# Kernel tuning notes

Measured on AMD Instinct MI355X. Metric: run time of the kernel, lower is better.

Reference implementation:

```python
import jax, jax.numpy as jnp
import numpy as np

B, N_PER, DEG = 1024, 256, 16
N = B * N_PER            # 262144 total nodes
E = B * N_PER * DEG      # 4194304 edges
F_IN, H, K, C = 7, 64, 50, 2


def setup_inputs() -> dict:
    key = jax.random.key(0)
    ks = jax.random.split(key, 16)
    rng = np.random.default_rng(0)
    # within-graph random edges: nodes of graph g occupy [g*N_PER, (g+1)*N_PER)
    offs = np.repeat(np.arange(B, dtype=np.int64) * N_PER, N_PER * DEG)
    src = offs + rng.integers(0, N_PER, size=E)
    dst = offs + rng.integers(0, N_PER, size=E)
    edge_index = jnp.asarray(np.stack([src, dst]), dtype=jnp.int64)
    batch = jnp.repeat(jnp.arange(B, dtype=jnp.int64), N_PER)
    sc = lambda fan: 1.0 / np.sqrt(fan)
    return {
        'x': jax.random.normal(ks[0], (N, F_IN), jnp.float32),
        'W1a': jax.random.normal(ks[1], (F_IN, H), jnp.float32) * sc(F_IN),
        'b1a': jnp.zeros((H,), jnp.float32),
        'W1b': jax.random.normal(ks[2], (H, H), jnp.float32) * sc(H),
        'b1b': jnp.zeros((H,), jnp.float32),
        'Wp': jax.random.normal(ks[3], (H, K), jnp.float32) * sc(H),
        'bp': jnp.zeros((K,), jnp.float32),
        'W2a': jax.random.normal(ks[4], (H, H), jnp.float32) * sc(H),
        'b2a': jnp.zeros((H,), jnp.float32),
        'W2b': jax.random.normal(ks[5], (H, H), jnp.float32) * sc(H),
        'b2b': jnp.zeros((H,), jnp.float32),
        'Wl': jax.random.normal(ks[6], (H, C), jnp.float32) * sc(H),
        'bl': jnp.zeros((C,), jnp.float32),
        'edge_index': edge_index,
        'batch': batch,
    }


def reference(x, W1a, b1a, W1b, b1b, Wp, bp, W2a, b2a, W2b, b2b, Wl, bl,
              edge_index, batch):
    src, dst = edge_index[0], edge_index[1]
    # --- sparse GINConv (eps=0): MLP(x + sum_{j in N(i)} x_j) ---
    agg = jnp.zeros_like(x).at[dst].add(x[src])          # scatter-add over edges
    h = jax.nn.relu((x + agg) @ W1a + b1a) @ W1b + b1b   # [N, H]
    # --- densify per graph (equal-size contiguous graphs) ---
    xd = h.reshape(B, N_PER, H)                          # [B, n, H]
    g = src // N_PER
    si = src % N_PER
    di = dst % N_PER
    A = jnp.zeros((B, N_PER, N_PER), x.dtype).at[g, si, di].add(1.0)
    # --- BNPool-style soft cluster pooling ---
    S = jax.nn.softmax(xd @ Wp + bp, axis=-1)            # [B, n, K]
    xp = jnp.einsum('bnk,bnd->bkd', S, xd)               # [B, K, H]
    AS = jnp.einsum('bnm,bmk->bnk', A, S)
    Ap = jnp.einsum('bnk,bnl->bkl', S, AS)               # [B, K, K]
    SSt = jnp.einsum('bnk,bmk->bnm', S, S)
    link_loss = jnp.sqrt(jnp.sum((A - SSt) ** 2)) / A.size
    ent_loss = -jnp.mean(jnp.sum(S * jnp.log(S + 1e-15), axis=-1))
    aux_loss = link_loss + ent_loss
    # --- DenseGINConv (eps=0): MLP(x + A @ x) ---
    h2 = xp + jnp.einsum('bkl,bld->bkd', Ap, xp)
    h2 = jax.nn.relu(h2 @ W2a + b2a) @ W2b + b2b         # [B, K, H]
    # --- mean pool over clusters + classifier ---
    logits = h2.mean(axis=1) @ Wl + bl                   # [B, C]
    return jax.nn.log_softmax(logits, axis=-1), aux_loss
```

## Files before the change

### kernel.cpp

```cpp
#include <hip/hip_runtime.h>
#include <math.h>

#define NG   1024
#define NP   256
#define EPG  4096
#define ETOT 4194304
#define NTOT (NG * NP)
#define FIN  7
#define HD   64
#define KC   50
#define CHK  64
#define FST  72
#define TSC  0.00390625f
#define TSCI 256.0f

#define SW_ST(k, n)  ((k) * 256 + ((n) ^ (((k) & 7) << 3)))
#define SW_AW(r, w)  ((r) * 128 + ((w) ^ (((r) & 7) << 2)))
#define SW_AH(r, h)  ((r) * 256 + ((h) ^ (((r) & 7) << 3)))


typedef __attribute__((ext_vector_type(8))) _Float16 v8h;
typedef __attribute__((ext_vector_type(4))) float v4f;

__device__ __align__(16) _Float16 g_W1bT[HD * HD];
__device__ __align__(16) _Float16 g_WWT[HD * HD];
__device__ __align__(16) _Float16 g_W2aT[HD * HD];
__device__ __align__(16) _Float16 g_W2bT[HD * HD];
__device__ float g_bP[HD];

__global__ void kw_conv(const float* __restrict__ W1b, const float* __restrict__ Wp,
                        const float* __restrict__ W2a, const float* __restrict__ W2b,
                        const float* __restrict__ b1b, const float* __restrict__ bp,
                        float* __restrict__ ws) {
    const int b = blockIdx.x, tid = threadIdx.x;
    if (b == 0 && tid < 4) ws[tid] = 0.f;
    {
        int i = b * 256 + tid;
        int d = i >> 6, j = i & 63;
        g_W1bT[i] = (_Float16)W1b[j * HD + d];
        g_W2aT[i] = (_Float16)W2a[j * HD + d];
        g_W2bT[i] = (_Float16)W2b[j * HD + d];
    }
    {
        int k = b * 4 + (tid >> 6), j = tid & 63;
        float acc = 0.f;
        if (k < KC) {
            for (int d = 0; d < HD; ++d)
                acc += W1b[j * HD + d] * Wp[d * KC + k];
        }
        g_WWT[k * HD + j] = (_Float16)acc;
    }
    if (tid < 4) {
        int k = b * 4 + tid;
        float a = 0.f;
        if (k < KC) {
            for (int d = 0; d < HD; ++d) a += b1b[d] * Wp[d * KC + k];
            a += bp[k];
        }
        g_bP[k] = a;
    }
}

__global__ void finalize_k(const float* __restrict__ ws, float* __restrict__ out) {
    if (threadIdx.x == 0) {
        float num = ws[0] - 2.f * ws[2] + ws[3];
        float link = sqrtf(fmaxf(num, 0.f)) / 67108864.0f;
        float ent  = -ws[1] / 262144.0f;
        out[2048] = link + ent;
    }
}

__device__ __forceinline__ float blockReduceN(float v, float* red, int nw) {
    __syncthreads();
    #pragma unroll
    for (int o = 32; o > 0; o >>= 1) v += __shfl_down(v, o);
    if ((threadIdx.x & 63) == 0) red[threadIdx.x >> 6] = v;
    __syncthreads();
    float r = 0.f;
    if (threadIdx.x == 0) {
        for (int i = 0; i < nw; ++i) r += red[i];
    }
    return r;
}

__launch_bounds__(1024, 2)
__global__ void mega(const int* __restrict__ esrc, const int* __restrict__ edst,
                     const float* __restrict__ x,
                     const float* __restrict__ W1a, const float* __restrict__ b1a,
                     const float* __restrict__ b1b,
                     const float* __restrict__ b2a, const float* __restrict__ b2b,
                     const float* __restrict__ Wl,  const float* __restrict__ bl,
                     float* __restrict__ out, float* __restrict__ ws)
{
    __shared__ __align__(16) _Float16 ST[64 * 256];
    __shared__ __align__(16) unsigned char aux[9216];
    __shared__ __align__(16) union {
        struct {
            unsigned char ssi[EPG];
            float xt8[NP * 8];
            unsigned int hist[256], cur[256], roff[NP + 1];
        } k1;
        struct {
            _Float16 t1b[CHK * FST];
            _Float16 t1T[CHK * FST];
            _Float16 Pf[CHK * FST];
        } k2;
        struct {
            unsigned int cnt[64 * 128];
        } a;
        struct {
            _Float16 Apf_tf[64 * FST];
            _Float16 xpT[64 * FST];
            _Float16 h2f[64 * FST];
        } b;
    } u;
    __shared__ float cs[64];
    __shared__ float red[16];

    float* xagg = (float*)aux;
    _Float16* T1T = (_Float16*)aux;

    const int g = blockIdx.x, tid = threadIdx.x;
    const int lane = tid & 63, wid = tid >> 6;
    const int l15 = lane & 15, quad = lane >> 4, fko = quad * 8;
    const int mt = (wid >> 2) << 4, nt = (wid & 3) << 4;

    for (int i = tid; i < 64 * 128; i += 1024) ((unsigned int*)ST)[i] = 0u;
    if (tid < 256) u.k1.hist[tid] = 0u;
    __syncthreads();

    unsigned int cellr[4];
    #pragma unroll
    for (int j = 0; j < 4; ++j) {
        int e = tid + j * 1024;
        int s = esrc[g * EPG + e] & (NP - 1);
        int d = edst[g * EPG + e] & (NP - 1);
        cellr[j] = (unsigned)((s << 8) | d);
        atomicAdd(&u.k1.hist[d], 1u);
    }
    for (int i = tid; i < NP * 8; i += 1024) {
        int n = i >> 3, f = i & 7;
        u.k1.xt8[i] = (f < FIN) ? x[g * NP * FIN + n * FIN + f] : 0.f;
    }
    __syncthreads();

    if (wid == 0) {
        unsigned carry = 0;
        for (int c = 0; c < 4; ++c) {
            unsigned v = u.k1.hist[c * 64 + lane];
            unsigned s = v;
            #pragma unroll
            for (int o = 1; o < 64; o <<= 1) {
                unsigned t = __shfl_up(s, o);
                if (lane >= o) s += t;
            }
            unsigned excl = s - v + carry;
            u.k1.roff[c * 64 + lane] = excl;
            u.k1.cur[c * 64 + lane] = excl;
            carry += __shfl(s, 63);
        }
        if (lane == 0) u.k1.roff[NP] = EPG;
    }
    __syncthreads();

    #pragma unroll
    for (int j = 0; j < 4; ++j) {
        unsigned c = cellr[j];
        unsigned p2 = atomicAdd(&u.k1.cur[c & 255u], 1u);
        u.k1.ssi[p2] = (unsigned char)(c >> 8);
    }
    __syncthreads();

    {
        const int gi = tid >> 3, f = tid & 7;
        for (int n = gi; n < NP; n += 128) {
            int beg = u.k1.roff[n], end = u.k1.roff[n + 1];
            float a = u.k1.xt8[n * 8 + f];
            for (int e = beg; e < end; ++e)
                a += u.k1.xt8[u.k1.ssi[e] * 8 + f];
            xagg[n * 8 + f] = a;
        }
    }
    __syncthreads();

    float entL = 0.f;
    v4f spa = {0.f, 0.f, 0.f, 0.f};
    {
        float w1r[FIN];
        #pragma unroll
        for (int f = 0; f < FIN; ++f) w1r[f] = W1a[f * HD + lane];
        float b1r = b1a[lane];

        for (int ch2 = 0; ch2 < 4; ++ch2) {
            const int rb = ch2 * 64;
            for (int n = wid; n < CHK; n += 16) {
                float a = b1r;
                #pragma unroll
                for (int f = 0; f < FIN; ++f) a += xagg[(rb + n) * 8 + f] * w1r[f];
                _Float16 tv = (_Float16)fmaxf(a, 0.f);
                u.k2.t1b[n * FST + lane] = tv;
                u.k2.t1T[lane * FST + n] = tv;
            }
            __syncthreads();

            {
                v4f acc = {0.f, 0.f, 0.f, 0.f};
                #pragma unroll
                for (int ks = 0; ks < 2; ++ks) {
                    v8h af = *(const v8h*)&u.k2.t1b[(mt + l15) * FST + ks * 32 + fko];
                    v8h bf = *(const v8h*)&g_WWT[(nt + l15) * HD + ks * 32 + fko];
                    acc = __builtin_amdgcn_mfma_f32_16x16x32_f16(af, bf, acc, 0, 0, 0);
                }
                int kcol = nt + l15;
                if (kcol < KC) {
                    float bv = g_bP[kcol];
                    #pragma unroll
                    for (int r = 0; r < 4; ++r)
                        u.k2.Pf[(mt + quad * 4 + r) * FST + kcol] =
                            (_Float16)(acc[r] + bv);
                }
            }
            __syncthreads();

            for (int n = wid; n < CHK; n += 16) {
                float a = (lane < KC) ? (float)u.k2.Pf[n * FST + lane] : -INFINITY;
                float m = a;
                #pragma unroll
                for (int o = 32; o > 0; o >>= 1) m = fmaxf(m, __shfl_xor(m, o));
                float e = __expf(a - m);
                float ss = e;
                #pragma unroll
                for (int o = 32; o > 0; o >>= 1) ss += __shfl_xor(ss, o);
                float s = e / ss;
                if (lane < KC) {
                    ST[SW_ST(lane, rb + n)] = (_Float16)s;
                    entL += s * __logf(s + 1e-15f);
                }
            }
            __syncthreads();

            {
                const int ar = mt + l15, br = nt + l15;
                #pragma unroll
                for (int ks = 0; ks < 2; ++ks) {
                    v8h af = *(const v8h*)&ST[SW_ST(ar, rb + ks * 32 + fko)];
                    v8h bf = *(const v8h*)&u.k2.t1T[br * FST + ks * 32 + fko];
                    spa = __builtin_amdgcn_mfma_f32_16x16x32_f16(af, bf, spa, 0, 0, 0);
                }
            }
            __syncthreads();
        }
    }

    {
        _Float16* SPb = u.k2.t1b;
        int c = nt + l15;
        #pragma unroll
        for (int r = 0; r < 4; ++r)
            SPb[(mt + quad * 4 + r) * FST + c] = (_Float16)spa[r];
    }
    {
        int k = tid >> 4, q = tid & 15;
        float v = 0.f;
        #pragma unroll
        for (int i = 0; i < 16; ++i) v += (float)ST[SW_ST(k, q * 16 + i)];
        #pragma unroll
        for (int o = 8; o > 0; o >>= 1) v += __shfl_xor(v, o);
        if (q == 0) cs[k] = v;
    }
    {
        float rE = blockReduceN(entL, red, 16);
        if (tid == 0) atomicAdd(&ws[1], rE);
    }

    v4f axp;
    {
        const int d = nt + l15;
        float bv = b1b[d];
        #pragma unroll
        for (int r = 0; r < 4; ++r) axp[r] = cs[mt + quad * 4 + r] * bv;
        #pragma unroll
        for (int ks = 0; ks < 2; ++ks) {
            v8h af = *(const v8h*)&u.k2.t1b[(mt + l15) * FST + ks * 32 + fko];
            v8h bf = *(const v8h*)&g_W1bT[(nt + l15) * HD + ks * 32 + fko];
            axp = __builtin_amdgcn_mfma_f32_16x16x32_f16(af, bf, axp, 0, 0, 0);
        }
    }
    __syncthreads();

    float sumA2 = 0.f;
    v4f ap = {0.f, 0.f, 0.f, 0.f};
    v4f ag = {0.f, 0.f, 0.f, 0.f};

    for (int ch = 0; ch < 4; ++ch) {
        for (int i = tid; i < 64 * 128; i += 1024) u.a.cnt[i] = 0u;
        __syncthreads();

        int rlo = ch << 6;
        #pragma unroll
        for (int j = 0; j < 4; ++j) {
            unsigned c = cellr[j];
            int sr = (int)(c >> 8) - rlo;
            if ((unsigned)sr < 64u) {
                int d = c & 255u;
                atomicAdd(&u.a.cnt[SW_AW(sr, d >> 1)],
                          (d & 1) ? 0x10000u : 1u);
            }
        }
        __syncthreads();

        for (int i = tid; i < 64 * 128; i += 1024) {
            unsigned v = u.a.cnt[i];
            float m0 = (float)(v & 0xffffu), m1 = (float)(v >> 16);
            sumA2 += m0 * m0 + m1 * m1;
            union { unsigned uu; _Float16 h[2]; } cv;
            cv.h[0] = (_Float16)m0; cv.h[1] = (_Float16)m1;
            u.a.cnt[i] = cv.uu;
        }
        __syncthreads();

        const _Float16* Af = (const _Float16*)u.a.cnt;

        {
            const int ar = mt + l15, br = nt + l15;
            v4f acc = {0.f, 0.f, 0.f, 0.f};
            #pragma unroll
            for (int ks = 0; ks < 8; ++ks) {
                v8h af = *(const v8h*)&Af[SW_AH(ar, ks * 32 + fko)];
                v8h bf = *(const v8h*)&ST[SW_ST(br, ks * 32 + fko)];
                acc = __builtin_amdgcn_mfma_f32_16x16x32_f16(af, bf, acc, 0, 0, 0);
            }
            int c = nt + l15;
            #pragma unroll
            for (int r = 0; r < 4; ++r)
                T1T[c * FST + mt + quad * 4 + r] = (_Float16)acc[r];
        }
        __syncthreads();

        {
            const int ar = mt + l15, br = nt + l15;
            #pragma unroll
            for (int ks = 0; ks < 2; ++ks) {
                int ko = (ch << 6) + ks * 32 + fko;
                v8h af = *(const v8h*)&ST[SW_ST(ar, ko)];
                v8h bt = *(const v8h*)&T1T[br * FST + ks * 32 + fko];
                v8h bs = *(const v8h*)&ST[SW_ST(br, ko)];
                ap = __builtin_amdgcn_mfma_f32_16x16x32_f16(af, bt, ap, 0, 0, 0);
                ag = __builtin_amdgcn_mfma_f32_16x16x32_f16(af, bs, ag, 0, 0, 0);
            }
        }
        __syncthreads();
    }

    float tr = 0.f, g2 = 0.f;
    {
        int c = nt + l15;
        #pragma unroll
        for (int r = 0; r < 4; ++r) {
            int k = mt + quad * 4 + r;
            u.b.Apf_tf[k * FST + c] = (_Float16)ap[r];
            u.b.xpT[c * FST + k] = (_Float16)axp[r];
            if (k < KC && c < KC) {
                if (k == c) tr += ap[r];
                g2 += ag[r] * ag[r];
            }
        }
    }

    float rA = blockReduceN(sumA2, red, 16);
    float rT = blockReduceN(tr, red, 16);
    float rG = blockReduceN(g2, red, 16);
    if (tid == 0) {
        atomicAdd(&ws[0], rA);
        atomicAdd(&ws[2], rT);
        atomicAdd(&ws[3], rG);
    }
    __syncthreads();

    {
        v4f hacc = axp;
        #pragma unroll
        for (int ks = 0; ks < 2; ++ks) {
            v8h af = *(const v8h*)&u.b.Apf_tf[(mt + l15) * FST + ks * 32 + fko];
            v8h bf = *(const v8h*)&u.b.xpT[(nt + l15) * FST + ks * 32 + fko];
            hacc = __builtin_amdgcn_mfma_f32_16x16x32_f16(af, bf, hacc, 0, 0, 0);
        }
        int d = nt + l15;
        #pragma unroll
        for (int r = 0; r < 4; ++r)
            u.b.h2f[(mt + quad * 4 + r) * FST + d] = (_Float16)(hacc[r] * TSC);
    }
    __syncthreads();

    {
        float bv = b2a[nt + l15] * TSC;
        v4f tacc = {bv, bv, bv, bv};
        #pragma unroll
        for (int ks = 0; ks < 2; ++ks) {
            v8h af = *(const v8h*)&u.b.h2f[(mt + l15) * FST + ks * 32 + fko];
            v8h bf = *(const v8h*)&g_W2aT[(nt + l15) * 64 + ks * 32 + fko];
            tacc = __builtin_amdgcn_mfma_f32_16x16x32_f16(af, bf, tacc, 0, 0, 0);
        }
        int d2 = nt + l15;
        #pragma unroll
        for (int r = 0; r < 4; ++r)
            u.b.Apf_tf[(mt + quad * 4 + r) * FST + d2] = (_Float16)fmaxf(tacc[r], 0.f);
    }
    __syncthreads();

    float l0 = 0.f, l1 = 0.f;
    {
        v4f oacc = {0.f, 0.f, 0.f, 0.f};
        #pragma unroll
        for (int ks = 0; ks < 2; ++ks) {
            v8h af = *(const v8h*)&u.b.Apf_tf[(mt + l15) * FST + ks * 32 + fko];
            v8h bf = *(const v8h*)&g_W2bT[(nt + l15) * 64 + ks * 32 + fko];
            oacc = __builtin_amdgcn_mfma_f32_16x16x32_f16(af, bf, oacc, 0, 0, 0);
        }
        int j = nt + l15;
        float bv = b2b[j];
        float wl0 = Wl[j * 2], wl1 = Wl[j * 2 + 1];
        #pragma unroll
        for (int r = 0; r < 4; ++r) {
            int k = mt + quad * 4 + r;
            if (k < KC) {
                float h3v = oacc[r] * TSCI + bv;
                l0 += h3v * wl0; l1 += h3v * wl1;
            }
        }
    }

    float rl0 = blockReduceN(l0, red, 16);
    float rl1 = blockReduceN(l1, red, 16);
    if (tid == 0) {
        float g0 = bl[0] + rl0 * (1.f / KC);
        float g1 = bl[1] + rl1 * (1.f / KC);
        float mm = fmaxf(g0, g1);
        float lse = mm + logf(expf(g0 - mm) + expf(g1 - mm));
        out[2 * g]     = g0 - lse;
        out[2 * g + 1] = g1 - lse;
    }
}

extern "C" void kernel_launch(void* const* d_in, const int* in_sizes, int n_in,
                              void* d_out, int out_size, void* d_ws, size_t ws_size,
                              hipStream_t stream) {
    const float* x    = (const float*)d_in[0];
    const float* W1a  = (const float*)d_in[1];
    const float* b1a  = (const float*)d_in[2];
    const float* W1b  = (const float*)d_in[3];
    const float* b1b  = (const float*)d_in[4];
    const float* Wp   = (const float*)d_in[5];
    const float* bp   = (const float*)d_in[6];
    const float* W2a  = (const float*)d_in[7];
    const float* b2a  = (const float*)d_in[8];
    const float* W2b  = (const float*)d_in[9];
    const float* b2b  = (const float*)d_in[10];
    const float* Wl   = (const float*)d_in[11];
    const float* bl   = (const float*)d_in[12];
    const int*   eidx = (const int*)d_in[13];
    float* out = (float*)d_out;
    float* ws  = (float*)d_ws;

    kw_conv<<<16, 256, 0, stream>>>(W1b, Wp, W2a, W2b, b1b, bp, ws);
    mega<<<NG, 1024, 0, stream>>>(eidx, eidx + ETOT, x,
                                  W1a, b1a, b1b,
                                  b2a, b2b, Wl, bl, out, ws);
    finalize_k<<<1, 64, 0, stream>>>(ws, out);
}
```

Measured before the change: 293.8 us.

## Halve A-chunk LDS, split-K T1 across waves, store xagg as fp16

The dense adjacency counting loop is restructured from 4 chunks of 64 source rows to 8 chunks of 32 rows. Each chunk's A·S product is split-K across two wave halves writing separate partial T1T buffers, and the two partials are summed by two MFMAs in the Ap accumulation step. Zeroing of the count buffer is folded into the end of each iteration, which removes one barrier per chunk. xagg is stored as fp16 in its own array. Together this shrinks LDS use, likely to allow more resident blocks or less LDS pressure, at the cost of more loop iterations and barriers and lower precision in the aggregated features.

```diff
diff --git a/kernel.cpp b/kernel.cpp
--- a/kernel.cpp
+++ b/kernel.cpp
@@ -93,7 +93,7 @@
                      float* __restrict__ out, float* __restrict__ ws)
 {
     __shared__ __align__(16) _Float16 ST[64 * 256];
-    __shared__ __align__(16) unsigned char aux[9216];
+    __shared__ __align__(16) _Float16 xagg[NP * 8];
     __shared__ __align__(16) union {
         struct {
             unsigned char ssi[EPG];
@@ -106,7 +106,8 @@
             _Float16 Pf[CHK * FST];
         } k2;
         struct {
-            unsigned int cnt[64 * 128];
+            unsigned int cnt[32 * 128];
+            _Float16 T1T[2][64 * 36];
         } a;
         struct {
             _Float16 Apf_tf[64 * FST];
@@ -117,13 +118,12 @@
     __shared__ float cs[64];
     __shared__ float red[16];
 
-    float* xagg = (float*)aux;
-    _Float16* T1T = (_Float16*)aux;
-
     const int g = blockIdx.x, tid = threadIdx.x;
     const int lane = tid & 63, wid = tid >> 6;
     const int l15 = lane & 15, quad = lane >> 4, fko = quad * 8;
     const int mt = (wid >> 2) << 4, nt = (wid & 3) << 4;
+    const int t8 = wid & 7, kh = wid >> 3;
+    const int mt2 = ((t8 >> 2) << 4), nt2 = ((t8 & 3) << 4);
 
     for (int i = tid; i < 64 * 128; i += 1024) ((unsigned int*)ST)[i] = 0u;
     if (tid < 256) u.k1.hist[tid] = 0u;
@@ -178,7 +178,7 @@
             float a = u.k1.xt8[n * 8 + f];
             for (int e = beg; e < end; ++e)
                 a += u.k1.xt8[u.k1.ssi[e] * 8 + f];
-            xagg[n * 8 + f] = a;
+            xagg[n * 8 + f] = (_Float16)a;
         }
     }
     __syncthreads();
@@ -196,7 +196,8 @@
             for (int n = wid; n < CHK; n += 16) {
                 float a = b1r;
                 #pragma unroll
-                for (int f = 0; f < FIN; ++f) a += xagg[(rb + n) * 8 + f] * w1r[f];
+                for (int f = 0; f < FIN; ++f)
+                    a += (float)xagg[(rb + n) * 8 + f] * w1r[f];
                 _Float16 tv = (_Float16)fmaxf(a, 0.f);
                 u.k2.t1b[n * FST + lane] = tv;
                 u.k2.t1T[lane * FST + n] = tv;
@@ -292,16 +293,16 @@
     v4f ap = {0.f, 0.f, 0.f, 0.f};
     v4f ag = {0.f, 0.f, 0.f, 0.f};
 
-    for (int ch = 0; ch < 4; ++ch) {
-        for (int i = tid; i < 64 * 128; i += 1024) u.a.cnt[i] = 0u;
-        __syncthreads();
-
-        int rlo = ch << 6;
+    for (int i = tid; i < 32 * 128; i += 1024) u.a.cnt[i] = 0u;
+    __syncthreads();
+
+    for (int ch = 0; ch < 8; ++ch) {
+        int rlo = ch << 5;
         #pragma unroll
         for (int j = 0; j < 4; ++j) {
             unsigned c = cellr[j];
             int sr = (int)(c >> 8) - rlo;
-            if ((unsigned)sr < 64u) {
+            if ((unsigned)sr < 32u) {
                 int d = c & 255u;
                 atomicAdd(&u.a.cnt[SW_AW(sr, d >> 1)],
                           (d & 1) ? 0x10000u : 1u);
@@ -309,7 +310,7 @@
         }
         __syncthreads();
 
-        for (int i = tid; i < 64 * 128; i += 1024) {
+        for (int i = tid; i < 32 * 128; i += 1024) {
             unsigned v = u.a.cnt[i];
             float m0 = (float)(v & 0xffffu), m1 = (float)(v >> 16);
             sumA2 += m0 * m0 + m1 * m1;
@@ -322,32 +323,33 @@
         const _Float16* Af = (const _Float16*)u.a.cnt;
 
         {
-            const int ar = mt + l15, br = nt + l15;
             v4f acc = {0.f, 0.f, 0.f, 0.f};
             #pragma unroll
-            for (int ks = 0; ks < 8; ++ks) {
-                v8h af = *(const v8h*)&Af[SW_AH(ar, ks * 32 + fko)];
-                v8h bf = *(const v8h*)&ST[SW_ST(br, ks * 32 + fko)];
+            for (int ks = 0; ks < 4; ++ks) {
+                int ko = kh * 128 + ks * 32 + fko;
+                v8h af = *(const v8h*)&Af[SW_AH(mt2 + l15, ko)];
+                v8h bf = *(const v8h*)&ST[SW_ST(nt2 + l15, ko)];
                 acc = __builtin_amdgcn_mfma_f32_16x16x32_f16(af, bf, acc, 0, 0, 0);
             }
-            int c = nt + l15;
+            int c = nt2 + l15;
             #pragma unroll
             for (int r = 0; r < 4; ++r)
-                T1T[c * FST + mt + quad * 4 + r] = (_Float16)acc[r];
+                u.a.T1T[kh][c * 36 + mt2 + quad * 4 + r] = (_Float16)acc[r];
         }
         __syncthreads();
 
         {
-            const int ar = mt + l15, br = nt + l15;
-            #pragma unroll
-            for (int ks = 0; ks < 2; ++ks) {
-                int ko = (ch << 6) + ks * 32 + fko;
-                v8h af = *(const v8h*)&ST[SW_ST(ar, ko)];
-                v8h bt = *(const v8h*)&T1T[br * FST + ks * 32 + fko];
-                v8h bs = *(const v8h*)&ST[SW_ST(br, ko)];
-                ap = __builtin_amdgcn_mfma_f32_16x16x32_f16(af, bt, ap, 0, 0, 0);
-                ag = __builtin_amdgcn_mfma_f32_16x16x32_f16(af, bs, ag, 0, 0, 0);
-            }
+            int ko = (ch << 5) + fko;
+            v8h af  = *(const v8h*)&ST[SW_ST(mt + l15, ko)];
+            v8h bt0 = *(const v8h*)&u.a.T1T[0][(nt + l15) * 36 + fko];
+            v8h bt1 = *(const v8h*)&u.a.T1T[1][(nt + l15) * 36 + fko];
+            v8h bs  = *(const v8h*)&ST[SW_ST(nt + l15, ko)];
+            ap = __builtin_amdgcn_mfma_f32_16x16x32_f16(af, bt0, ap, 0, 0, 0);
+            ap = __builtin_amdgcn_mfma_f32_16x16x32_f16(af, bt1, ap, 0, 0, 0);
+            ag = __builtin_amdgcn_mfma_f32_16x16x32_f16(af, bs, ag, 0, 0, 0);
+        }
+        if (ch < 7) {
+            for (int i = tid; i < 32 * 128; i += 1024) u.a.cnt[i] = 0u;
         }
         __syncthreads();
     }
```

Result: slower. 304.1 us (+3.5%).

## Replace dense adjacency build and A@S MFMA with sparse CSR gather by source

Applied to the files above, without the earlier changes.

Instead of materialising the dense 256x256 adjacency in four chunks and multiplying it by S with MFMA, the kernel builds a second CSR keyed by source node and computes A@S by gathering S rows along edges. sum(A^2) is rebuilt from duplicate-edge counts within each destination list (E + 2*pairs), which drops the dense count pass. xagg is stored in fp16 and launch bounds drop to one block per CU, because the new shared buffers (Srows and others) raise LDS use. This trades dense tensor-core work and atomics for irregular gathers, an O(deg^2) duplicate count, and fewer resident blocks.

```diff
diff --git a/kernel.cpp b/kernel.cpp
--- a/kernel.cpp
+++ b/kernel.cpp
@@ -15,8 +15,6 @@
 #define TSCI 256.0f
 
 #define SW_ST(k, n)  ((k) * 256 + ((n) ^ (((k) & 7) << 3)))
-#define SW_AW(r, w)  ((r) * 128 + ((w) ^ (((r) & 7) << 2)))
-#define SW_AH(r, h)  ((r) * 256 + ((h) ^ (((r) & 7) << 3)))
 
 
 typedef __attribute__((ext_vector_type(8))) _Float16 v8h;
@@ -83,7 +81,7 @@
     return r;
 }
 
-__launch_bounds__(1024, 2)
+__launch_bounds__(1024, 1)
 __global__ void mega(const int* __restrict__ esrc, const int* __restrict__ edst,
                      const float* __restrict__ x,
                      const float* __restrict__ W1a, const float* __restrict__ b1a,
@@ -93,12 +91,16 @@
                      float* __restrict__ out, float* __restrict__ ws)
 {
     __shared__ __align__(16) _Float16 ST[64 * 256];
-    __shared__ __align__(16) unsigned char aux[9216];
+    __shared__ __align__(16) _Float16 Srows[NP * HD];
+    __shared__ __align__(16) _Float16 xagg[NP * 8];
+    __shared__ unsigned char sdi[EPG];
+    __shared__ unsigned int roffs[NP + 1];
     __shared__ __align__(16) union {
         struct {
             unsigned char ssi[EPG];
             float xt8[NP * 8];
-            unsigned int hist[256], cur[256], roff[NP + 1];
+            unsigned int hist_di[256], cur_di[256], cur_si[256];
+            unsigned int roff_di[NP + 1];
         } k1;
         struct {
             _Float16 t1b[CHK * FST];
@@ -106,7 +108,7 @@
             _Float16 Pf[CHK * FST];
         } k2;
         struct {
-            unsigned int cnt[64 * 128];
+            _Float16 AST[64 * 256];
         } a;
         struct {
             _Float16 Apf_tf[64 * FST];
@@ -117,68 +119,93 @@
     __shared__ float cs[64];
     __shared__ float red[16];
 
-    float* xagg = (float*)aux;
-    _Float16* T1T = (_Float16*)aux;
-
     const int g = blockIdx.x, tid = threadIdx.x;
     const int lane = tid & 63, wid = tid >> 6;
     const int l15 = lane & 15, quad = lane >> 4, fko = quad * 8;
     const int mt = (wid >> 2) << 4, nt = (wid & 3) << 4;
 
     for (int i = tid; i < 64 * 128; i += 1024) ((unsigned int*)ST)[i] = 0u;
-    if (tid < 256) u.k1.hist[tid] = 0u;
-    __syncthreads();
-
-    unsigned int cellr[4];
-    #pragma unroll
-    for (int j = 0; j < 4; ++j) {
-        int e = tid + j * 1024;
-        int s = esrc[g * EPG + e] & (NP - 1);
-        int d = edst[g * EPG + e] & (NP - 1);
-        cellr[j] = (unsigned)((s << 8) | d);
-        atomicAdd(&u.k1.hist[d], 1u);
-    }
-    for (int i = tid; i < NP * 8; i += 1024) {
-        int n = i >> 3, f = i & 7;
-        u.k1.xt8[i] = (f < FIN) ? x[g * NP * FIN + n * FIN + f] : 0.f;
-    }
-    __syncthreads();
-
-    if (wid == 0) {
-        unsigned carry = 0;
-        for (int c = 0; c < 4; ++c) {
-            unsigned v = u.k1.hist[c * 64 + lane];
-            unsigned s = v;
-            #pragma unroll
-            for (int o = 1; o < 64; o <<= 1) {
-                unsigned t = __shfl_up(s, o);
-                if (lane >= o) s += t;
-            }
-            unsigned excl = s - v + carry;
-            u.k1.roff[c * 64 + lane] = excl;
-            u.k1.cur[c * 64 + lane] = excl;
-            carry += __shfl(s, 63);
-        }
-        if (lane == 0) u.k1.roff[NP] = EPG;
-    }
-    __syncthreads();
-
-    #pragma unroll
-    for (int j = 0; j < 4; ++j) {
-        unsigned c = cellr[j];
-        unsigned p2 = atomicAdd(&u.k1.cur[c & 255u], 1u);
-        u.k1.ssi[p2] = (unsigned char)(c >> 8);
-    }
-    __syncthreads();
-
+    if (tid < 256) { u.k1.hist_di[tid] = 0u; u.k1.cur_si[tid] = 0u; }
+    __syncthreads();
+
+    {
+        unsigned int cellr[4];
+        #pragma unroll
+        for (int j = 0; j < 4; ++j) {
+            int e = tid + j * 1024;
+            int s = esrc[g * EPG + e] & (NP - 1);
+            int d = edst[g * EPG + e] & (NP - 1);
+            cellr[j] = (unsigned)((s << 8) | d);
+            atomicAdd(&u.k1.hist_di[d], 1u);
+            atomicAdd(&u.k1.cur_si[s], 1u);
+        }
+        for (int i = tid; i < NP * 8; i += 1024) {
+            int n = i >> 3, f = i & 7;
+            u.k1.xt8[i] = (f < FIN) ? x[g * NP * FIN + n * FIN + f] : 0.f;
+        }
+        __syncthreads();
+
+        if (wid == 0) {
+            unsigned carry = 0;
+            for (int c = 0; c < 4; ++c) {
+                unsigned v = u.k1.hist_di[c * 64 + lane];
+                unsigned s = v;
+                #pragma unroll
+                for (int o = 1; o < 64; o <<= 1) {
+                    unsigned t = __shfl_up(s, o);
+                    if (lane >= o) s += t;
+                }
+                unsigned excl = s - v + carry;
+                u.k1.roff_di[c * 64 + lane] = excl;
+                u.k1.cur_di[c * 64 + lane] = excl;
+                carry += __shfl(s, 63);
+            }
+            if (lane == 0) u.k1.roff_di[NP] = EPG;
+        } else if (wid == 1) {
+            unsigned carry = 0;
+            for (int c = 0; c < 4; ++c) {
+                unsigned v = u.k1.cur_si[c * 64 + lane];
+                unsigned s = v;
+                #pragma unroll
+                for (int o = 1; o < 64; o <<= 1) {
+                    unsigned t = __shfl_up(s, o);
+                    if (lane >= o) s += t;
+                }
+                unsigned excl = s - v + carry;
+                roffs[c * 64 + lane] = excl;
+                u.k1.cur_si[c * 64 + lane] = excl;
+                carry += __shfl(s, 63);
+            }
+            if (lane == 0) roffs[NP] = EPG;
+        }
+        __syncthreads();
+
+        #pragma unroll
+        for (int j = 0; j < 4; ++j) {
+            unsigned c = cellr[j];
+            unsigned s = c >> 8, d = c & 255u;
+            unsigned p = atomicAdd(&u.k1.cur_di[d], 1u);
+            u.k1.ssi[p] = (unsigned char)s;
+            unsigned q = atomicAdd(&u.k1.cur_si[s], 1u);
+            sdi[q] = (unsigned char)d;
+        }
+        __syncthreads();
+    }
+
+    float eqL = 0.f;
     {
         const int gi = tid >> 3, f = tid & 7;
         for (int n = gi; n < NP; n += 128) {
-            int beg = u.k1.roff[n], end = u.k1.roff[n + 1];
+            int beg = u.k1.roff_di[n], end = u.k1.roff_di[n + 1];
             float a = u.k1.xt8[n * 8 + f];
             for (int e = beg; e < end; ++e)
                 a += u.k1.xt8[u.k1.ssi[e] * 8 + f];
-            xagg[n * 8 + f] = a;
+            xagg[n * 8 + f] = (_Float16)a;
+            for (int i = beg; i < end; ++i) {
+                int v = u.k1.ssi[i];
+                for (int jj = i + 1 + f; jj < end; jj += 8)
+                    eqL += (u.k1.ssi[jj] == v) ? 1.f : 0.f;
+            }
         }
     }
     __syncthreads();
@@ -196,7 +223,8 @@
             for (int n = wid; n < CHK; n += 16) {
                 float a = b1r;
                 #pragma unroll
-                for (int f = 0; f < FIN; ++f) a += xagg[(rb + n) * 8 + f] * w1r[f];
+                for (int f = 0; f < FIN; ++f)
+                    a += (float)xagg[(rb + n) * 8 + f] * w1r[f];
                 _Float16 tv = (_Float16)fmaxf(a, 0.f);
                 u.k2.t1b[n * FST + lane] = tv;
                 u.k2.t1T[lane * FST + n] = tv;
@@ -232,6 +260,7 @@
                 #pragma unroll
                 for (int o = 32; o > 0; o >>= 1) ss += __shfl_xor(ss, o);
                 float s = e / ss;
+                Srows[(rb + n) * HD + lane] = (_Float16)s;
                 if (lane < KC) {
                     ST[SW_ST(lane, rb + n)] = (_Float16)s;
                     entL += s * __logf(s + 1e-15f);
@@ -288,69 +317,32 @@
     }
     __syncthreads();
 
-    float sumA2 = 0.f;
+    for (int si = wid; si < NP; si += 16) {
+        int beg = roffs[si], end = roffs[si + 1];
+        float acc = 0.f;
+        for (int e = beg; e < end; ++e) {
+            int d = sdi[e];
+            acc += (float)Srows[d * HD + lane];
+        }
+        u.a.AST[SW_ST(lane, si)] = (_Float16)acc;
+    }
+    __syncthreads();
+
     v4f ap = {0.f, 0.f, 0.f, 0.f};
     v4f ag = {0.f, 0.f, 0.f, 0.f};
-
-    for (int ch = 0; ch < 4; ++ch) {
-        for (int i = tid; i < 64 * 128; i += 1024) u.a.cnt[i] = 0u;
-        __syncthreads();
-
-        int rlo = ch << 6;
-        #pragma unroll
-        for (int j = 0; j < 4; ++j) {
-            unsigned c = cellr[j];
-            int sr = (int)(c >> 8) - rlo;
-            if ((unsigned)sr < 64u) {
-                int d = c & 255u;
-                atomicAdd(&u.a.cnt[SW_AW(sr, d >> 1)],
-                          (d & 1) ? 0x10000u : 1u);
-            }
-        }
-        __syncthreads();
-
-        for (int i = tid; i < 64 * 128; i += 1024) {
-            unsigned v = u.a.cnt[i];
-            float m0 = (float)(v & 0xffffu), m1 = (float)(v >> 16);
-            sumA2 += m0 * m0 + m1 * m1;
-            union { unsigned uu; _Float16 h[2]; } cv;
-            cv.h[0] = (_Float16)m0; cv.h[1] = (_Float16)m1;
-            u.a.cnt[i] = cv.uu;
-        }
-        __syncthreads();
-
-        const _Float16* Af = (const _Float16*)u.a.cnt;
-
-        {
-            const int ar = mt + l15, br = nt + l15;
-            v4f acc = {0.f, 0.f, 0.f, 0.f};
-            #pragma unroll
-            for (int ks = 0; ks < 8; ++ks) {
-                v8h af = *(const v8h*)&Af[SW_AH(ar, ks * 32 + fko)];
-                v8h bf = *(const v8h*)&ST[SW_ST(br, ks * 32 + fko)];
-                acc = __builtin_amdgcn_mfma_f32_16x16x32_f16(af, bf, acc, 0, 0, 0);
-            }
-            int c = nt + l15;
-            #pragma unroll
-            for (int r = 0; r < 4; ++r)
-                T1T[c * FST + mt + quad * 4 + r] = (_Float16)acc[r];
-        }
-        __syncthreads();
-
-        {
-            const int ar = mt + l15, br = nt + l15;
-            #pragma unroll
-            for (int ks = 0; ks < 2; ++ks) {
-                int ko = (ch << 6) + ks * 32 + fko;
-                v8h af = *(const v8h*)&ST[SW_ST(ar, ko)];
-                v8h bt = *(const v8h*)&T1T[br * FST + ks * 32 + fko];
-                v8h bs = *(const v8h*)&ST[SW_ST(br, ko)];
-                ap = __builtin_amdgcn_mfma_f32_16x16x32_f16(af, bt, ap, 0, 0, 0);
-                ag = __builtin_amdgcn_mfma_f32_16x16x32_f16(af, bs, ag, 0, 0, 0);
-            }
-        }
-        __syncthreads();
-    }
+    {
+        const int ar = mt + l15, br = nt + l15;
+        #pragma unroll
+        for (int ks = 0; ks < 8; ++ks) {
+            int ko = ks * 32 + fko;
+            v8h af = *(const v8h*)&ST[SW_ST(ar, ko)];
+            v8h bt = *(const v8h*)&u.a.AST[SW_ST(br, ko)];
+            v8h bs = *(const v8h*)&ST[SW_ST(br, ko)];
+            ap = __builtin_amdgcn_mfma_f32_16x16x32_f16(af, bt, ap, 0, 0, 0);
+            ag = __builtin_amdgcn_mfma_f32_16x16x32_f16(af, bs, ag, 0, 0, 0);
+        }
+    }
+    __syncthreads();
 
     float tr = 0.f, g2 = 0.f;
     {
@@ -367,11 +359,11 @@
         }
     }
 
-    float rA = blockReduceN(sumA2, red, 16);
+    float rA = blockReduceN(eqL, red, 16);
     float rT = blockReduceN(tr, red, 16);
     float rG = blockReduceN(g2, red, 16);
     if (tid == 0) {
-        atomicAdd(&ws[0], rA);
+        atomicAdd(&ws[0], 4096.f + 2.f * rA);
         atomicAdd(&ws[2], rT);
         atomicAdd(&ws[3], rG);
     }
```

New measurement: 376.9 us. +28.3%, slower.

## Process all 256 nodes in one pass and compute softmax from MFMA registers

Applied to the files above, without the earlier changes.

The four 64-row chunk loop for the first MLP, projection, softmax and S^T·h product is replaced by a single pass over all 256 nodes, with a larger transposed buffer. The softmax and entropy now run directly on the MFMA accumulator registers using 16-lane shuffles, so the Pf staging buffer and several block barriers are gone, and the entropy term is rewritten as s*(p-m) - log Z. The aggregated features are stored as fp16, and the paired block reductions are merged into one three-value reduction. The larger shared-memory footprint forces launch bounds down to one block per CU, which lowers occupancy.

```diff
diff --git a/kernel.cpp b/kernel.cpp
--- a/kernel.cpp
+++ b/kernel.cpp
@@ -5,12 +5,11 @@
 #define NP   256
 #define EPG  4096
 #define ETOT 4194304
-#define NTOT (NG * NP)
 #define FIN  7
 #define HD   64
 #define KC   50
-#define CHK  64
 #define FST  72
+#define TST  264
 #define TSC  0.00390625f
 #define TSCI 256.0f
 
@@ -83,7 +82,30 @@
     return r;
 }
 
-__launch_bounds__(1024, 2)
+__device__ __forceinline__ void blockReduce3(float& a, float& b, float& c,
+                                             float* red) {
+    __syncthreads();
+    #pragma unroll
+    for (int o = 32; o > 0; o >>= 1) {
+        a += __shfl_down(a, o);
+        b += __shfl_down(b, o);
+        c += __shfl_down(c, o);
+    }
+    const int wid = threadIdx.x >> 6;
+    if ((threadIdx.x & 63) == 0) {
+        red[wid * 3] = a; red[wid * 3 + 1] = b; red[wid * 3 + 2] = c;
+    }
+    __syncthreads();
+    if (threadIdx.x == 0) {
+        float ra = 0.f, rb = 0.f, rc = 0.f;
+        for (int i = 0; i < 16; ++i) {
+            ra += red[i * 3]; rb += red[i * 3 + 1]; rc += red[i * 3 + 2];
+        }
+        a = ra; b = rb; c = rc;
+    }
+}
+
+__launch_bounds__(1024, 1)
 __global__ void mega(const int* __restrict__ esrc, const int* __restrict__ edst,
                      const float* __restrict__ x,
                      const float* __restrict__ W1a, const float* __restrict__ b1a,
@@ -93,7 +115,7 @@
                      float* __restrict__ out, float* __restrict__ ws)
 {
     __shared__ __align__(16) _Float16 ST[64 * 256];
-    __shared__ __align__(16) unsigned char aux[9216];
+    __shared__ __align__(16) _Float16 xagg[NP * 8];
     __shared__ __align__(16) union {
         struct {
             unsigned char ssi[EPG];
@@ -101,12 +123,12 @@
             unsigned int hist[256], cur[256], roff[NP + 1];
         } k1;
         struct {
-            _Float16 t1b[CHK * FST];
-            _Float16 t1T[CHK * FST];
-            _Float16 Pf[CHK * FST];
+            _Float16 t1b[NP * FST];
+            _Float16 t1T[HD * TST];
         } k2;
         struct {
             unsigned int cnt[64 * 128];
+            _Float16 T1T[64 * FST];
         } a;
         struct {
             _Float16 Apf_tf[64 * FST];
@@ -115,10 +137,7 @@
         } b;
     } u;
     __shared__ float cs[64];
-    __shared__ float red[16];
-
-    float* xagg = (float*)aux;
-    _Float16* T1T = (_Float16*)aux;
+    __shared__ float red[48];
 
     const int g = blockIdx.x, tid = threadIdx.x;
     const int lane = tid & 63, wid = tid >> 6;
@@ -178,80 +197,94 @@
             float a = u.k1.xt8[n * 8 + f];
             for (int e = beg; e < end; ++e)
                 a += u.k1.xt8[u.k1.ssi[e] * 8 + f];
-            xagg[n * 8 + f] = a;
-        }
-    }
-    __syncthreads();
-
-    float entL = 0.f;
-    v4f spa = {0.f, 0.f, 0.f, 0.f};
+            xagg[n * 8 + f] = (_Float16)a;
+        }
+    }
+    __syncthreads();
+
     {
         float w1r[FIN];
         #pragma unroll
         for (int f = 0; f < FIN; ++f) w1r[f] = W1a[f * HD + lane];
         float b1r = b1a[lane];
-
-        for (int ch2 = 0; ch2 < 4; ++ch2) {
-            const int rb = ch2 * 64;
-            for (int n = wid; n < CHK; n += 16) {
-                float a = b1r;
-                #pragma unroll
-                for (int f = 0; f < FIN; ++f) a += xagg[(rb + n) * 8 + f] * w1r[f];
-                _Float16 tv = (_Float16)fmaxf(a, 0.f);
-                u.k2.t1b[n * FST + lane] = tv;
-                u.k2.t1T[lane * FST + n] = tv;
-            }
-            __syncthreads();
-
-            {
-                v4f acc = {0.f, 0.f, 0.f, 0.f};
-                #pragma unroll
-                for (int ks = 0; ks < 2; ++ks) {
-                    v8h af = *(const v8h*)&u.k2.t1b[(mt + l15) * FST + ks * 32 + fko];
-                    v8h bf = *(const v8h*)&g_WWT[(nt + l15) * HD + ks * 32 + fko];
-                    acc = __builtin_amdgcn_mfma_f32_16x16x32_f16(af, bf, acc, 0, 0, 0);
+        for (int it = 0; it < 16; ++it) {
+            int n = it * 16 + wid;
+            float a = b1r;
+            #pragma unroll
+            for (int f = 0; f < FIN; ++f)
+                a += (float)xagg[n * 8 + f] * w1r[f];
+            _Float16 tv = (_Float16)fmaxf(a, 0.f);
+            u.k2.t1b[n * FST + lane] = tv;
+            u.k2.t1T[lane * TST + n] = tv;
+        }
+    }
+    __syncthreads();
+
+    float entL = 0.f;
+    {
+        const int r16 = wid << 4;
+        v4f pa[4];
+        #pragma unroll
+        for (int c = 0; c < 4; ++c) {
+            v4f acc = {0.f, 0.f, 0.f, 0.f};
+            #pragma unroll
+            for (int ks = 0; ks < 2; ++ks) {
+                v8h af = *(const v8h*)&u.k2.t1b[(r16 + l15) * FST + ks * 32 + fko];
+                v8h bf = *(const v8h*)&g_WWT[(c * 16 + l15) * HD + ks * 32 + fko];
+                acc = __builtin_amdgcn_mfma_f32_16x16x32_f16(af, bf, acc, 0, 0, 0);
+            }
+            pa[c] = acc;
+        }
+        float bv[4]; bool valid[4];
+        #pragma unroll
+        for (int c = 0; c < 4; ++c) {
+            int col = c * 16 + l15;
+            bv[c] = g_bP[col];
+            valid[c] = col < KC;
+        }
+        #pragma unroll
+        for (int r = 0; r < 4; ++r) {
+            float pv[4];
+            #pragma unroll
+            for (int c = 0; c < 4; ++c)
+                pv[c] = valid[c] ? (pa[c][r] + bv[c]) : -INFINITY;
+            float m = fmaxf(fmaxf(pv[0], pv[1]), fmaxf(pv[2], pv[3]));
+            #pragma unroll
+            for (int o = 8; o > 0; o >>= 1) m = fmaxf(m, __shfl_xor(m, o));
+            float e[4], Z = 0.f;
+            #pragma unroll
+            for (int c = 0; c < 4; ++c) {
+                e[c] = valid[c] ? __expf(pv[c] - m) : 0.f;
+                Z += e[c];
+            }
+            #pragma unroll
+            for (int o = 8; o > 0; o >>= 1) Z += __shfl_xor(Z, o);
+            float zi = 1.f / Z, lZ = __logf(Z);
+            int row = r16 + quad * 4 + r;
+            #pragma unroll
+            for (int c = 0; c < 4; ++c) {
+                if (valid[c]) {
+                    float s = e[c] * zi;
+                    ST[SW_ST(c * 16 + l15, row)] = (_Float16)s;
+                    entL += s * (pv[c] - m);
                 }
-                int kcol = nt + l15;
-                if (kcol < KC) {
-                    float bv = g_bP[kcol];
-                    #pragma unroll
-                    for (int r = 0; r < 4; ++r)
-                        u.k2.Pf[(mt + quad * 4 + r) * FST + kcol] =
-                            (_Float16)(acc[r] + bv);
-                }
-            }
-            __syncthreads();
-
-            for (int n = wid; n < CHK; n += 16) {
-                float a = (lane < KC) ? (float)u.k2.Pf[n * FST + lane] : -INFINITY;
-                float m = a;
-                #pragma unroll
-                for (int o = 32; o > 0; o >>= 1) m = fmaxf(m, __shfl_xor(m, o));
-                float e = __expf(a - m);
-                float ss = e;
-                #pragma unroll
-                for (int o = 32; o > 0; o >>= 1) ss += __shfl_xor(ss, o);
-                float s = e / ss;
-                if (lane < KC) {
-                    ST[SW_ST(lane, rb + n)] = (_Float16)s;
-                    entL += s * __logf(s + 1e-15f);
-                }
-            }
-            __syncthreads();
-
-            {
-                const int ar = mt + l15, br = nt + l15;
-                #pragma unroll
-                for (int ks = 0; ks < 2; ++ks) {
-                    v8h af = *(const v8h*)&ST[SW_ST(ar, rb + ks * 32 + fko)];
-                    v8h bf = *(const v8h*)&u.k2.t1T[br * FST + ks * 32 + fko];
-                    spa = __builtin_amdgcn_mfma_f32_16x16x32_f16(af, bf, spa, 0, 0, 0);
-                }
-            }
-            __syncthreads();
-        }
-    }
-
+            }
+            if (l15 == 0) entL -= lZ;
+        }
+    }
+    __syncthreads();
+
+    v4f spa = {0.f, 0.f, 0.f, 0.f};
+    {
+        const int ar = mt + l15, br = nt + l15;
+        #pragma unroll
+        for (int ks = 0; ks < 8; ++ks) {
+            int ko = ks * 32 + fko;
+            v8h af = *(const v8h*)&ST[SW_ST(ar, ko)];
+            v8h bf = *(const v8h*)&u.k2.t1T[br * TST + ko];
+            spa = __builtin_amdgcn_mfma_f32_16x16x32_f16(af, bf, spa, 0, 0, 0);
+        }
+    }
     {
         _Float16* SPb = u.k2.t1b;
         int c = nt + l15;
@@ -333,7 +366,7 @@
             int c = nt + l15;
             #pragma unroll
             for (int r = 0; r < 4; ++r)
-                T1T[c * FST + mt + quad * 4 + r] = (_Float16)acc[r];
+                u.a.T1T[c * FST + mt + quad * 4 + r] = (_Float16)acc[r];
         }
         __syncthreads();
 
@@ -343,7 +376,7 @@
             for (int ks = 0; ks < 2; ++ks) {
                 int ko = (ch << 6) + ks * 32 + fko;
                 v8h af = *(const v8h*)&ST[SW_ST(ar, ko)];
-                v8h bt = *(const v8h*)&T1T[br * FST + ks * 32 + fko];
+                v8h bt = *(const v8h*)&u.a.T1T[br * FST + ks * 32 + fko];
                 v8h bs = *(const v8h*)&ST[SW_ST(br, ko)];
                 ap = __builtin_amdgcn_mfma_f32_16x16x32_f16(af, bt, ap, 0, 0, 0);
                 ag = __builtin_amdgcn_mfma_f32_16x16x32_f16(af, bs, ag, 0, 0, 0);
@@ -367,13 +400,11 @@
         }
     }
 
-    float rA = blockReduceN(sumA2, red, 16);
-    float rT = blockReduceN(tr, red, 16);
-    float rG = blockReduceN(g2, red, 16);
+    blockReduce3(sumA2, tr, g2, red);
     if (tid == 0) {
-        atomicAdd(&ws[0], rA);
-        atomicAdd(&ws[2], rT);
-        atomicAdd(&ws[3], rG);
+        atomicAdd(&ws[0], sumA2);
+        atomicAdd(&ws[2], tr);
+        atomicAdd(&ws[3], g2);
     }
     __syncthreads();
 
@@ -430,11 +461,11 @@
         }
     }
 
-    float rl0 = blockReduceN(l0, red, 16);
-    float rl1 = blockReduceN(l1, red, 16);
+    float dummy = 0.f;
+    blockReduce3(l0, l1, dummy, red);
     if (tid == 0) {
-        float g0 = bl[0] + rl0 * (1.f / KC);
-        float g1 = bl[1] + rl1 * (1.f / KC);
+        float g0 = bl[0] + l0 * (1.f / KC);
+        float g1 = bl[1] + l1 * (1.f / KC);
         float mm = fmaxf(g0, g1);
         float lse = mm + logf(expf(g0 - mm) + expf(g1 - mm));
         out[2 * g]     = g0 - lse;
```

Result: faster. 254.8 us (-13.3%).
